# Kernel optimization log

Hardware: AMD Instinct MI355X
Metric: run time of the kernel (lower is better)

The kernel has to match this reference:

```python
import jax, jax.numpy as jnp
from jax import lax
import numpy as np

D = 1024   # hidden_size
N = 8      # num_experts
K = 2      # num_chosen_experts
KS = 1     # num_shared_experts
H = 2 * D  # hidden_ratio * D
B, S = 2, 1024


def setup_inputs() -> dict:
    key = jax.random.key(0)
    k1, k2, k3, k4 = jax.random.split(key, 4)
    scale = 1.0 / np.sqrt(D).astype(np.float32)
    x = jax.random.normal(k1, (B, S, D), dtype=jnp.float32)
    Wg = jax.random.normal(k2, (D, N), dtype=jnp.float32) * scale
    Wl1 = jax.random.normal(k3, (N, D, 2 * H), dtype=jnp.float32) * scale
    Wl2 = jax.random.normal(k4, (N, H, D), dtype=jnp.float32) * scale
    return {"x_BSD": x, "Wg_DN": Wg, "Wl1_ND2H": Wl1, "Wl2_NHD": Wl2}


def _moe(x_BSD, Wg_DN, Wl1_ND2H, Wl2_NHD):
    b, s, d = x_BSD.shape
    x_MD = x_BSD.reshape(b * s, d)            # [M, D]
    Nr = N - KS                               # number of routed experts

    # --- gating (softmax path) ---
    s_raw_MN = x_MD @ Wg_DN                   # [M, N]
    routed = jax.nn.softmax(s_raw_MN[:, :Nr].astype(jnp.float32), axis=-1)
    shared = jax.nn.softmax(s_raw_MN[:, Nr:].astype(jnp.float32), axis=-1)

    # biases for routed experts are zero at init -> topk on raw softmax scores
    _, idx_MK = lax.top_k(routed, K - KS)     # [M, K-KS]
    mask = jnp.sum(jax.nn.one_hot(idx_MK, Nr, dtype=jnp.float32), axis=1)  # [M, Nr]
    sel = routed * mask
    routed_n = sel / jnp.sum(sel, axis=-1, keepdims=True)   # renormalize selected gates
    shared_n = shared / jnp.sum(shared, axis=-1, keepdims=True)
    gates_MN = jnp.concatenate([routed_n, shared_n], axis=-1).astype(x_MD.dtype)  # [M, N]

    # --- experts: gather-free dense combine; gates are exactly 0 for unselected experts ---
    def step(y_MD, inp):
        w1_D2H, w2_HD, g_M = inp
        z = x_MD @ w1_D2H                     # [M, 2H]
        a, bgate = jnp.split(z, 2, axis=-1)
        h = jax.nn.silu(bgate) * a            # SwiGLU
        return y_MD + g_M[:, None] * (h @ w2_HD), None

    y0 = jnp.zeros_like(x_MD)
    y_MD, _ = lax.scan(step, y0, (Wl1_ND2H, Wl2_NHD, gates_MN.T))
    return y_MD.reshape(b, s, d)


def reference(x_BSD, Wg_DN, Wl1_ND2H, Wl2_NHD):
    return _moe(x_BSD, Wg_DN, Wl1_ND2H, Wl2_NHD)
```

## Files before the change

kernel.cpp:

```cpp
#include <hip/hip_runtime.h>
#include <stdint.h>


typedef __bf16 bf16x8 __attribute__((ext_vector_type(8)));
typedef float f32x4 __attribute__((ext_vector_type(4)));

typedef __attribute__((address_space(1))) const void gvoid_t;
typedef __attribute__((address_space(3))) void lvoid_t;

__device__ __forceinline__ void gload16(void* lds, const void* g) {
  __builtin_amdgcn_global_load_lds((gvoid_t*)g, (lvoid_t*)lds, 16, 0, 0);
}

__device__ __forceinline__ uint16_t f2bf(float f) {
  union { float f; uint32_t u; } v; v.f = f;
  uint32_t u = v.u + 0x7fffu + ((v.u >> 16) & 1u);
  return (uint16_t)(u >> 16);
}

#define S_VMCNT12() asm volatile("s_waitcnt vmcnt(12)" ::: "memory")
#define S_VMCNT0()  asm volatile("s_waitcnt vmcnt(0)" ::: "memory")
#define S_LGKM0()   asm volatile("s_waitcnt lgkmcnt(0)" ::: "memory")
#define S_BAR()     __builtin_amdgcn_s_barrier()

#define CVT_PK(dst, lo, hi) \
  asm("v_cvt_pk_bf16_f32 %0, %1, %2" : "=v"(dst) : "v"(lo), "v"(hi))

__global__ __launch_bounds__(256) void gate_kernel(const float* __restrict__ x,
                                                   const float* __restrict__ Wg,
                                                   uint16_t* __restrict__ xbf,
                                                   int* __restrict__ idx) {
  int wid = threadIdx.x >> 6, lane = threadIdx.x & 63;
  int m = blockIdx.x * 4 + wid;
  const float* xr = x + (size_t)m * 1024;
  uint16_t* xbr = xbf + (size_t)m * 1024;
  float acc[8] = {0.f, 0.f, 0.f, 0.f, 0.f, 0.f, 0.f, 0.f};
  for (int it = 0; it < 4; ++it) {
    int dbase = it * 256 + lane * 4;
    float4 xv = *reinterpret_cast<const float4*>(xr + dbase);
    ushort4 o;
    o.x = f2bf(xv.x); o.y = f2bf(xv.y); o.z = f2bf(xv.z); o.w = f2bf(xv.w);
    *reinterpret_cast<ushort4*>(xbr + dbase) = o;
    const float* xp = reinterpret_cast<const float*>(&xv);
    for (int dd = 0; dd < 4; ++dd) {
      float xs = xp[dd];
      float4 w0 = *reinterpret_cast<const float4*>(Wg + (size_t)(dbase + dd) * 8);
      float4 w1 = *reinterpret_cast<const float4*>(Wg + (size_t)(dbase + dd) * 8 + 4);
      acc[0] += xs * w0.x; acc[1] += xs * w0.y; acc[2] += xs * w0.z; acc[3] += xs * w0.w;
      acc[4] += xs * w1.x; acc[5] += xs * w1.y; acc[6] += xs * w1.z; acc[7] += xs * w1.w;
    }
  }
  for (int j = 0; j < 7; ++j)
    for (int off = 32; off; off >>= 1)
      acc[j] += __shfl_xor(acc[j], off);
  if (lane == 0) {
    int best = 0; float bv = acc[0];
    for (int j = 1; j < 7; ++j) if (acc[j] > bv) { bv = acc[j]; best = j; }
    idx[m] = best;
  }
}

__global__ __launch_bounds__(256) void compact_kernel(const int* __restrict__ idx,
                                                      int* __restrict__ soff,
                                                      int* __restrict__ scnt,
                                                      int* __restrict__ rowmap,
                                                      int* __restrict__ tokrow) {
  __shared__ int hist[256][7];
  __shared__ int cnts[7];
  __shared__ int off[7];
  int t = threadIdx.x;
  int e8[8];
  int lh[7] = {0, 0, 0, 0, 0, 0, 0};
#pragma unroll
  for (int i = 0; i < 8; ++i) { int e = idx[t * 8 + i]; e8[i] = e; lh[e]++; }
#pragma unroll
  for (int e = 0; e < 7; ++e) hist[t][e] = lh[e];
  __syncthreads();
  if (t < 7) {
    int run = 0;
    for (int i = 0; i < 256; ++i) { int v = hist[i][t]; hist[i][t] = run; run += v; }
    cnts[t] = run;
  }
  __syncthreads();
  if (t == 0) {
    int run = 0;
    for (int e = 0; e < 7; ++e) { off[e] = run; soff[e] = run; scnt[e] = cnts[e]; run += cnts[e]; }
    soff[7] = 0; scnt[7] = 2048;
  }
  __syncthreads();
  int pos[7];
#pragma unroll
  for (int e = 0; e < 7; ++e) pos[e] = off[e] + hist[t][e];
#pragma unroll
  for (int i = 0; i < 8; ++i) {
    int m = t * 8 + i, e = e8[i];
    int r = pos[e]++;
    rowmap[r] = m;
    tokrow[m] = r;
  }
}

__global__ __launch_bounds__(256, 2) void ffn1_kernel(
    const uint16_t* __restrict__ xbf,
    const float* __restrict__ W1,
    const int* __restrict__ soff, const int* __restrict__ scnt,
    const int* __restrict__ rowmap,
    uint16_t* __restrict__ h)
{
  int by = blockIdx.y;
  int seg, rt;
  if (by < 42) { seg = by / 6; rt = by % 6; } else { seg = 7; rt = by - 42; }
  int cnt = scnt[seg];
  if (rt * 128 >= cnt) return;
  int base = (seg == 7) ? 2048 : soff[seg];
  int rbase = (seg == 7) ? 0 : soff[seg];
  int n0 = blockIdx.x * 64;

  __shared__ uint16_t lds[2][16384];

  int t = threadIdx.x, lane = t & 63, w = t >> 6;
  int trow = w * 8 + ((t >> 3) & 7);
  int slot = (t & 7) ^ (trow & 7);

  const uint16_t* aptr[4];
#pragma unroll
  for (int i = 0; i < 4; ++i) {
    int rl = i * 32 + trow;
    int rr = rt * 128 + rl; if (rr >= cnt) rr = cnt - 1;
    int tok = (seg == 7) ? rr : rowmap[rbase + rr];
    aptr[i] = xbf + (size_t)tok * 1024 + slot * 8;
  }
  auto stageA = [&](int buf, int kt) {
    uint16_t* L = lds[buf];
#pragma unroll
    for (int i = 0; i < 4; ++i) gload16(&L[(i * 32 + trow) * 64 + (t & 7) * 8], aptr[i] + kt * 64);
  };

  const float* w1f = W1 + (size_t)seg * (1024u * 4096u);
  int kg = t >> 5;
  int n4 = (t & 31) * 4;
  int gcol = (n4 < 64) ? (n0 + n4) : (2048 + n0 + n4 - 64);
  const float* bsrc = w1f + (size_t)(kg * 8) * 4096 + gcol;
  int bwoff[4];
#pragma unroll
  for (int j = 0; j < 4; ++j) {
    int cl = n4 + j;
    int sw = cl ^ ((cl >> 2) & 7);
    bwoff[j] = 8192 + kg * 1024 + sw * 8;
  }
  f32x4 breg[8];
  auto issueB = [&](int kt) {
    const float* p = bsrc + (size_t)kt * 64 * 4096;
#pragma unroll
    for (int i = 0; i < 8; ++i) breg[i] = *reinterpret_cast<const f32x4*>(p + (size_t)i * 4096);
  };
  auto writeB = [&](int buf) {
    uint16_t* L = lds[buf];
#pragma unroll
    for (int j = 0; j < 4; ++j) {
      uint32_t p0, p1, p2, p3;
      CVT_PK(p0, breg[0][j], breg[1][j]);
      CVT_PK(p1, breg[2][j], breg[3][j]);
      CVT_PK(p2, breg[4][j], breg[5][j]);
      CVT_PK(p3, breg[6][j], breg[7][j]);
      uint4 v; v.x = p0; v.y = p1; v.z = p2; v.w = p3;
      *reinterpret_cast<uint4*>(&L[bwoff[j]]) = v;
    }
  };

  int wr = (w >> 1) & 1, wc = w & 1;
  int l15 = lane & 15, lk = lane >> 4;
  int boffA[2], boffB[2];
#pragma unroll
  for (int n = 0; n < 2; ++n) {
    int cl = wc * 32 + n * 16 + l15;
    boffA[n] = 8192 + (cl ^ ((cl >> 2) & 7)) * 8;
    cl += 64;
    boffB[n] = 8192 + (cl ^ ((cl >> 2) & 7)) * 8;
  }

  f32x4 acca[4][2] = {};
  f32x4 accb[4][2] = {};

  issueB(0); stageA(0, 0);
  writeB(0);
  issueB(1); stageA(1, 1);
  S_LGKM0();

  for (int kt = 0; kt < 16; ++kt) {
    if (kt < 15) S_VMCNT12(); else S_VMCNT0();
    S_BAR();
    const uint16_t* L = lds[kt & 1];
#pragma unroll
    for (int g = 0; g < 2; ++g) {
      __builtin_amdgcn_s_setprio(1);
      bf16x8 af[4];
#pragma unroll
      for (int m = 0; m < 4; ++m) {
        int row = wr * 64 + m * 16 + l15;
        int p = (g * 4 + lk) ^ (row & 7);
        af[m] = *reinterpret_cast<const bf16x8*>(&L[row * 64 + p * 8]);
      }
#pragma unroll
      for (int n = 0; n < 2; ++n) {
        int ks = (g * 4 + lk) * 1024;
        bf16x8 ba = *reinterpret_cast<const bf16x8*>(&L[boffA[n] + ks]);
        bf16x8 bb = *reinterpret_cast<const bf16x8*>(&L[boffB[n] + ks]);
#pragma unroll
        for (int m = 0; m < 4; ++m) {
          acca[m][n] = __builtin_amdgcn_mfma_f32_16x16x32_bf16(af[m], ba, acca[m][n], 0, 0, 0);
          accb[m][n] = __builtin_amdgcn_mfma_f32_16x16x32_bf16(af[m], bb, accb[m][n], 0, 0, 0);
        }
      }
      __builtin_amdgcn_s_setprio(0);
    }
    if (kt < 15) writeB((kt + 1) & 1);
    S_LGKM0();
    S_BAR();
    if (kt < 14) { issueB(kt + 2); stageA(kt & 1, kt + 2); }
  }

#pragma unroll
  for (int m = 0; m < 4; ++m)
#pragma unroll
    for (int n = 0; n < 2; ++n) {
      int col = n0 + wc * 32 + n * 16 + l15;
#pragma unroll
      for (int j = 0; j < 4; ++j) {
        int row = rt * 128 + wr * 64 + m * 16 + lk * 4 + j;
        if (row < cnt) {
          float a = acca[m][n][j], b = accb[m][n][j];
          float sv = b / (1.0f + __expf(-b));
          h[(size_t)(base + row) * 2048 + col] = f2bf(sv * a);
        }
      }
    }
}

__global__ __launch_bounds__(256, 2) void ffn2_kernel(
    const uint16_t* __restrict__ h,
    const float* __restrict__ W2,
    const int* __restrict__ soff, const int* __restrict__ scnt,
    float* __restrict__ y,
    float* __restrict__ yr)
{
  int by = blockIdx.y;
  int seg, rt;
  if (by < 42) { seg = by / 6; rt = by % 6; } else { seg = 7; rt = by - 42; }
  int cnt = scnt[seg];
  if (rt * 128 >= cnt) return;
  int base = (seg == 7) ? 2048 : soff[seg];
  int obase = (seg == 7) ? 0 : soff[seg];
  int n0 = blockIdx.x * 128;

  __shared__ uint16_t lds[2][16384];

  int t = threadIdx.x, lane = t & 63, w = t >> 6;
  int trow = w * 8 + ((t >> 3) & 7);
  int slot = (t & 7) ^ (trow & 7);

  const uint16_t* aptr[4];
#pragma unroll
  for (int i = 0; i < 4; ++i) {
    int rl = i * 32 + trow;
    int rr = rt * 128 + rl; if (rr >= cnt) rr = cnt - 1;
    aptr[i] = h + (size_t)(base + rr) * 2048 + slot * 8;
  }
  auto stageA = [&](int buf, int kt) {
    uint16_t* L = lds[buf];
#pragma unroll
    for (int i = 0; i < 4; ++i) gload16(&L[(i * 32 + trow) * 64 + (t & 7) * 8], aptr[i] + kt * 64);
  };

  const float* w2f = W2 + (size_t)seg * (2048u * 1024u);
  int kg = t >> 5;
  int n4 = (t & 31) * 4;
  const float* bsrc = w2f + (size_t)(kg * 8) * 1024 + n0 + n4;
  int bwoff[4];
#pragma unroll
  for (int j = 0; j < 4; ++j) {
    int cl = n4 + j;
    int sw = cl ^ ((cl >> 2) & 7);
    bwoff[j] = 8192 + kg * 1024 + sw * 8;
  }
  f32x4 breg[8];
  auto issueB = [&](int kt) {
    const float* p = bsrc + (size_t)kt * 64 * 1024;
#pragma unroll
    for (int i = 0; i < 8; ++i) breg[i] = *reinterpret_cast<const f32x4*>(p + (size_t)i * 1024);
  };
  auto writeB = [&](int buf) {
    uint16_t* L = lds[buf];
#pragma unroll
    for (int j = 0; j < 4; ++j) {
      uint32_t p0, p1, p2, p3;
      CVT_PK(p0, breg[0][j], breg[1][j]);
      CVT_PK(p1, breg[2][j], breg[3][j]);
      CVT_PK(p2, breg[4][j], breg[5][j]);
      CVT_PK(p3, breg[6][j], breg[7][j]);
      uint4 v; v.x = p0; v.y = p1; v.z = p2; v.w = p3;
      *reinterpret_cast<uint4*>(&L[bwoff[j]]) = v;
    }
  };

  int wr = (w >> 1) & 1, wc = w & 1;
  int l15 = lane & 15, lk = lane >> 4;
  int boff[4];
#pragma unroll
  for (int n = 0; n < 4; ++n) {
    int cl = wc * 64 + n * 16 + l15;
    boff[n] = 8192 + (cl ^ ((cl >> 2) & 7)) * 8;
  }

  f32x4 acc[4][4] = {};

  issueB(0); stageA(0, 0);
  writeB(0);
  issueB(1); stageA(1, 1);
  S_LGKM0();

  for (int kt = 0; kt < 32; ++kt) {
    if (kt < 31) S_VMCNT12(); else S_VMCNT0();
    S_BAR();
    const uint16_t* L = lds[kt & 1];
#pragma unroll
    for (int g = 0; g < 2; ++g) {
      __builtin_amdgcn_s_setprio(1);
      bf16x8 af[4];
#pragma unroll
      for (int m = 0; m < 4; ++m) {
        int row = wr * 64 + m * 16 + l15;
        int p = (g * 4 + lk) ^ (row & 7);
        af[m] = *reinterpret_cast<const bf16x8*>(&L[row * 64 + p * 8]);
      }
#pragma unroll
      for (int n = 0; n < 4; ++n) {
        bf16x8 bfr = *reinterpret_cast<const bf16x8*>(&L[boff[n] + (g * 4 + lk) * 1024]);
#pragma unroll
        for (int m = 0; m < 4; ++m)
          acc[m][n] = __builtin_amdgcn_mfma_f32_16x16x32_bf16(af[m], bfr, acc[m][n], 0, 0, 0);
      }
      __builtin_amdgcn_s_setprio(0);
    }
    if (kt < 31) writeB((kt + 1) & 1);
    S_LGKM0();
    S_BAR();
    if (kt < 30) { issueB(kt + 2); stageA(kt & 1, kt + 2); }
  }

#pragma unroll
  for (int m = 0; m < 4; ++m)
#pragma unroll
    for (int n = 0; n < 4; ++n) {
      int col = n0 + wc * 64 + n * 16 + l15;
#pragma unroll
      for (int j = 0; j < 4; ++j) {
        int row = rt * 128 + wr * 64 + m * 16 + lk * 4 + j;
        if (row < cnt) {
          if (seg == 7) y[(size_t)row * 1024 + col] = acc[m][n][j];
          else          yr[(size_t)(obase + row) * 1024 + col] = acc[m][n][j];
        }
      }
    }
}

__global__ __launch_bounds__(256) void combine_kernel(const float* __restrict__ yr,
                                                      const int* __restrict__ tokrow,
                                                      float* __restrict__ y) {
  int m = blockIdx.x;
  int d = threadIdx.x * 4;
  int r = tokrow[m];
  float4 a = *reinterpret_cast<const float4*>(yr + (size_t)r * 1024 + d);
  float4 o = *reinterpret_cast<const float4*>(y + (size_t)m * 1024 + d);
  o.x += a.x; o.y += a.y; o.z += a.z; o.w += a.w;
  *reinterpret_cast<float4*>(y + (size_t)m * 1024 + d) = o;
}

extern "C" void kernel_launch(void* const* d_in, const int* in_sizes, int n_in,
                              void* d_out, int out_size, void* d_ws, size_t ws_size,
                              hipStream_t stream)
{
  const float* x   = (const float*)d_in[0];
  const float* Wg  = (const float*)d_in[1];
  const float* Wl1 = (const float*)d_in[2];
  const float* Wl2 = (const float*)d_in[3];
  float* y = (float*)d_out;
  char* ws = (char*)d_ws;

  uint16_t* xbf = (uint16_t*)(ws);
  uint16_t* h   = (uint16_t*)(ws + (4ull  << 20));
  float*    yr  = (float*)   (ws + (20ull << 20));
  int* idx    = (int*)(ws + (28ull << 20));
  int* tokrow = idx + 2048;
  int* soff   = tokrow + 2048;
  int* scnt   = soff + 8;
  int* rowmap = scnt + 8;

  gate_kernel<<<512, 256, 0, stream>>>(x, Wg, xbf, idx);
  compact_kernel<<<1, 256, 0, stream>>>(idx, soff, scnt, rowmap, tokrow);
  ffn1_kernel<<<dim3(32, 58), 256, 0, stream>>>(xbf, Wl1, soff, scnt, rowmap, h);
  ffn2_kernel<<<dim3(8, 58), 256, 0, stream>>>(h, Wl2, soff, scnt, y, yr);
  combine_kernel<<<2048, 256, 0, stream>>>(yr, tokrow, y);
}
```

Baseline: 131.1 us.

## Double-buffer B weight registers to prefetch fp32 weights two tiles ahead

Both expert GEMM kernels now keep two register sets for the fp32 weight tiles, so global loads for tile kt+3 are issued while tile kt+1 is converted and written to LDS. The main loop is unrolled by two to alternate between the register sets. The aim is to hide more global-memory latency on the weight stream, which is read as fp32 and converted to bf16. In exchange it uses 32 more VGPRs per thread, which may lower occupancy, and the vmcnt wait counts must stay correct.

```diff
diff --git a/kernel.cpp b/kernel.cpp
--- a/kernel.cpp
+++ b/kernel.cpp
@@ -19,6 +19,7 @@
 }
 
 #define S_VMCNT12() asm volatile("s_waitcnt vmcnt(12)" ::: "memory")
+#define S_VMCNT16() asm volatile("s_waitcnt vmcnt(16)" ::: "memory")
 #define S_VMCNT0()  asm volatile("s_waitcnt vmcnt(0)" ::: "memory")
 #define S_LGKM0()   asm volatile("s_waitcnt lgkmcnt(0)" ::: "memory")
 #define S_BAR()     __builtin_amdgcn_s_barrier()
@@ -148,22 +149,22 @@
     int sw = cl ^ ((cl >> 2) & 7);
     bwoff[j] = 8192 + kg * 1024 + sw * 8;
   }
-  f32x4 breg[8];
-  auto issueB = [&](int kt) {
+  f32x4 P0[8], P1[8];
+  auto issueB = [&](f32x4 (&P)[8], int kt) {
     const float* p = bsrc + (size_t)kt * 64 * 4096;
 #pragma unroll
-    for (int i = 0; i < 8; ++i) breg[i] = *reinterpret_cast<const f32x4*>(p + (size_t)i * 4096);
-  };
-  auto writeB = [&](int buf) {
+    for (int i = 0; i < 8; ++i) P[i] = *reinterpret_cast<const f32x4*>(p + (size_t)i * 4096);
+  };
+  auto writeB = [&](f32x4 (&P)[8], int buf) {
     uint16_t* L = lds[buf];
 #pragma unroll
     for (int j = 0; j < 4; ++j) {
-      uint32_t p0, p1, p2, p3;
-      CVT_PK(p0, breg[0][j], breg[1][j]);
-      CVT_PK(p1, breg[2][j], breg[3][j]);
-      CVT_PK(p2, breg[4][j], breg[5][j]);
-      CVT_PK(p3, breg[6][j], breg[7][j]);
-      uint4 v; v.x = p0; v.y = p1; v.z = p2; v.w = p3;
+      uint32_t q0, q1, q2, q3;
+      CVT_PK(q0, P[0][j], P[1][j]);
+      CVT_PK(q1, P[2][j], P[3][j]);
+      CVT_PK(q2, P[4][j], P[5][j]);
+      CVT_PK(q3, P[6][j], P[7][j]);
+      uint4 v; v.x = q0; v.y = q1; v.z = q2; v.w = q3;
       *reinterpret_cast<uint4*>(&L[bwoff[j]]) = v;
     }
   };
@@ -182,15 +183,8 @@
   f32x4 acca[4][2] = {};
   f32x4 accb[4][2] = {};
 
-  issueB(0); stageA(0, 0);
-  writeB(0);
-  issueB(1); stageA(1, 1);
-  S_LGKM0();
-
-  for (int kt = 0; kt < 16; ++kt) {
-    if (kt < 15) S_VMCNT12(); else S_VMCNT0();
-    S_BAR();
-    const uint16_t* L = lds[kt & 1];
+  auto compute = [&](int buf) {
+    const uint16_t* L = lds[buf];
 #pragma unroll
     for (int g = 0; g < 2; ++g) {
       __builtin_amdgcn_s_setprio(1);
@@ -214,10 +208,33 @@
       }
       __builtin_amdgcn_s_setprio(0);
     }
-    if (kt < 15) writeB((kt + 1) & 1);
-    S_LGKM0();
+  };
+
+  const int NT = 16;
+  issueB(P0, 0); stageA(0, 0);
+  issueB(P1, 1); stageA(1, 1);
+  S_VMCNT16();
+  writeB(P0, 0);
+  issueB(P0, 2);
+  S_LGKM0();
+
+#pragma unroll 1
+  for (int kt = 0; kt < NT; kt += 2) {
+    if (kt < NT - 2) S_VMCNT12(); else S_VMCNT0();
     S_BAR();
-    if (kt < 14) { issueB(kt + 2); stageA(kt & 1, kt + 2); }
+    compute(0);
+    if (kt < NT - 1) writeB(P1, 1);
+    S_LGKM0(); S_BAR();
+    if (kt < NT - 3) issueB(P1, kt + 3);
+    if (kt < NT - 2) stageA(0, kt + 2);
+    int ko = kt + 1;
+    if (ko < NT - 2) S_VMCNT12(); else S_VMCNT0();
+    S_BAR();
+    compute(1);
+    if (ko < NT - 1) writeB(P0, 0);
+    S_LGKM0(); S_BAR();
+    if (ko < NT - 3) issueB(P0, ko + 3);
+    if (ko < NT - 2) stageA(1, ko + 2);
   }
 
 #pragma unroll
@@ -283,22 +300,22 @@
     int sw = cl ^ ((cl >> 2) & 7);
     bwoff[j] = 8192 + kg * 1024 + sw * 8;
   }
-  f32x4 breg[8];
-  auto issueB = [&](int kt) {
+  f32x4 P0[8], P1[8];
+  auto issueB = [&](f32x4 (&P)[8], int kt) {
     const float* p = bsrc + (size_t)kt * 64 * 1024;
 #pragma unroll
-    for (int i = 0; i < 8; ++i) breg[i] = *reinterpret_cast<const f32x4*>(p + (size_t)i * 1024);
-  };
-  auto writeB = [&](int buf) {
+    for (int i = 0; i < 8; ++i) P[i] = *reinterpret_cast<const f32x4*>(p + (size_t)i * 1024);
+  };
+  auto writeB = [&](f32x4 (&P)[8], int buf) {
     uint16_t* L = lds[buf];
 #pragma unroll
     for (int j = 0; j < 4; ++j) {
-      uint32_t p0, p1, p2, p3;
-      CVT_PK(p0, breg[0][j], breg[1][j]);
-      CVT_PK(p1, breg[2][j], breg[3][j]);
-      CVT_PK(p2, breg[4][j], breg[5][j]);
-      CVT_PK(p3, breg[6][j], breg[7][j]);
-      uint4 v; v.x = p0; v.y = p1; v.z = p2; v.w = p3;
+      uint32_t q0, q1, q2, q3;
+      CVT_PK(q0, P[0][j], P[1][j]);
+      CVT_PK(q1, P[2][j], P[3][j]);
+      CVT_PK(q2, P[4][j], P[5][j]);
+      CVT_PK(q3, P[6][j], P[7][j]);
+      uint4 v; v.x = q0; v.y = q1; v.z = q2; v.w = q3;
       *reinterpret_cast<uint4*>(&L[bwoff[j]]) = v;
     }
   };
@@ -314,15 +331,8 @@
 
   f32x4 acc[4][4] = {};
 
-  issueB(0); stageA(0, 0);
-  writeB(0);
-  issueB(1); stageA(1, 1);
-  S_LGKM0();
-
-  for (int kt = 0; kt < 32; ++kt) {
-    if (kt < 31) S_VMCNT12(); else S_VMCNT0();
-    S_BAR();
-    const uint16_t* L = lds[kt & 1];
+  auto compute = [&](int buf) {
+    const uint16_t* L = lds[buf];
 #pragma unroll
     for (int g = 0; g < 2; ++g) {
       __builtin_amdgcn_s_setprio(1);
@@ -342,10 +352,33 @@
       }
       __builtin_amdgcn_s_setprio(0);
     }
-    if (kt < 31) writeB((kt + 1) & 1);
-    S_LGKM0();
+  };
+
+  const int NT = 32;
+  issueB(P0, 0); stageA(0, 0);
+  issueB(P1, 1); stageA(1, 1);
+  S_VMCNT16();
+  writeB(P0, 0);
+  issueB(P0, 2);
+  S_LGKM0();
+
+#pragma unroll 1
+  for (int kt = 0; kt < NT; kt += 2) {
+    if (kt < NT - 2) S_VMCNT12(); else S_VMCNT0();
     S_BAR();
-    if (kt < 30) { issueB(kt + 2); stageA(kt & 1, kt + 2); }
+    compute(0);
+    if (kt < NT - 1) writeB(P1, 1);
+    S_LGKM0(); S_BAR();
+    if (kt < NT - 3) issueB(P1, kt + 3);
+    if (kt < NT - 2) stageA(0, kt + 2);
+    int ko = kt + 1;
+    if (ko < NT - 2) S_VMCNT12(); else S_VMCNT0();
+    S_BAR();
+    compute(1);
+    if (ko < NT - 1) writeB(P0, 0);
+    S_LGKM0(); S_BAR();
+    if (ko < NT - 3) issueB(P0, ko + 3);
+    if (ko < NT - 2) stageA(1, ko + 2);
   }
 
 #pragma unroll
```

New measurement: 129.4 us. About the same (-1.3%).
